# Kernel tuning notes

Measured on AMD Instinct MI355X. Metric: run time of the kernel, lower is better.

The kernel has to match this reference:

```python
import jax, jax.numpy as jnp
import numpy as np

B, H, W = 32, 128, 128
NA = 9            # number of anchors
STRIDE = 16.0
CLS_THRESH = 0.95
MAX_IOU = 0.1
NUM_PROP = 10
NEG = -1e9        # sentinel for suppressed / below-threshold scores


def setup_inputs() -> dict:
    key = jax.random.key(0)
    inputs = jax.random.normal(key, (B, H, W, NA * 4 + NA + 1), dtype=jnp.float32)
    anchors = jnp.array([[0.5, 32.0], [1.0, 32.0], [2.0, 32.0],
                         [0.5, 64.0], [1.0, 64.0], [2.0, 64.0],
                         [0.5, 128.0], [1.0, 128.0], [2.0, 128.0]], dtype=jnp.float32)
    return {"inputs": inputs, "anchors": anchors}


def _decode(inputs, anchors):
    b, h, w, c = inputs.shape
    cls = inputs[..., -1]
    # zero out 1-pixel border (the tf.pad'ed cancel matrix)
    border = jnp.zeros((h, w), inputs.dtype).at[1:-1, 1:-1].set(1.0)
    cls = cls * border
    a_reg = inputs[..., -10:-1]           # [B,H,W,9]
    bbox_reg = inputs[..., :-10]          # [B,H,W,36]
    a_idx = jnp.argmax(a_reg, axis=-1)    # [B,H,W] best anchor per position
    # gather the 4 deltas of the chosen anchor: channels a_idx*4 .. a_idx*4+3
    gidx = a_idx[..., None] * 4 + jnp.arange(4)
    deltas = jnp.take_along_axis(bbox_reg, gidx, axis=-1)          # [B,H,W,4]
    anc = anchors[a_idx].astype(jnp.float32)                       # [B,H,W,2]
    # anchor box: center x from column, center y from row, height=anc[:,1], width=anc[:,1]/anc[:,0]
    ax = (jnp.arange(w, dtype=jnp.float32)[None, :] + 0.5) * STRIDE  # [1,W]
    ay = (jnp.arange(h, dtype=jnp.float32)[:, None] + 0.5) * STRIDE  # [H,1]
    a0 = jnp.broadcast_to(ax, (h, w))[None]                          # [1,H,W]
    a1 = jnp.broadcast_to(ay, (h, w))[None]
    a2 = anc[..., 1]
    a3 = anc[..., 1] / anc[..., 0]
    b0 = deltas[..., 0] * a2 + a0
    b1 = deltas[..., 1] * a3 + a1
    b2 = jnp.exp(deltas[..., 2]) * a2
    b3 = jnp.exp(deltas[..., 3]) * a3
    bboxes = jnp.stack([b0, b1, b2, b3], axis=-1)                    # [B,H,W,4]
    coords = jnp.stack([b1 - b3 / 2, b0 - b2 / 2,
                        b1 + b3 / 2, b0 + b2 / 2], axis=-1)          # [y1,x1,y2,x2]
    scores = jnp.where(cls > CLS_THRESH, cls, NEG)                   # mask below-threshold
    n = h * w
    return (bboxes.reshape(b, n, 4), coords.reshape(b, n, 4), scores.reshape(b, n))


def _nms_one(boxes, coords, scores):
    # greedy NMS, equivalent to tf.image.non_max_suppression over the valid candidates
    n = scores.shape[0]
    area = jnp.maximum(coords[:, 2] - coords[:, 0], 0.0) * jnp.maximum(coords[:, 3] - coords[:, 1], 0.0)
    idx_range = jnp.arange(n)

    def body(i, state):
        sc, out = state
        j = jnp.argmax(sc)
        ok = sc[j] > NEG / 2
        sel = coords[j]
        iy1 = jnp.maximum(coords[:, 0], sel[0])
        ix1 = jnp.maximum(coords[:, 1], sel[1])
        iy2 = jnp.minimum(coords[:, 2], sel[2])
        ix2 = jnp.minimum(coords[:, 3], sel[3])
        inter = jnp.maximum(iy2 - iy1, 0.0) * jnp.maximum(ix2 - ix1, 0.0)
        area_s = jnp.maximum(sel[2] - sel[0], 0.0) * jnp.maximum(sel[3] - sel[1], 0.0)
        iou = inter / (area + area_s - inter + 1e-10)
        suppress = (iou > MAX_IOU) | (idx_range == j)
        sc = jnp.where(ok & suppress, NEG, sc)
        out = out.at[i].set(jnp.where(ok, boxes[j], jnp.zeros(4, boxes.dtype)))
        return sc, out

    out0 = jnp.zeros((NUM_PROP, 4), boxes.dtype)
    _, out = jax.lax.fori_loop(0, NUM_PROP, body, (scores, out0))
    return out


def _forward(inputs, anchors):
    bboxes, coords, scores = _decode(inputs, anchors)
    return jax.vmap(_nms_one)(bboxes, coords, scores)   # [B, NUM_PROP, 4]


def reference(inputs, anchors):
    return _forward(inputs, anchors)
```

## Files before the change

kernel.cpp:

```cpp
#include <hip/hip_runtime.h>
#include <math.h>

#define BB 32
#define HH 128
#define WW 128
#define NA 9
#define CCH 46
#define NPIX (HH*WW)
#define STRIDE_F 16.0f
#define CLS_T 0.95f
#define MAX_IOU_F 0.1f
#define NUM_PROP 10
#define NEGV -1000000000.0f

#define TILE_PIX 256
#define TILE_FLOATS (TILE_PIX * CCH)
#define TILE_VEC (TILE_FLOATS / 4)

#define NSHARD 8
#define NREG (BB * NSHARD)
#define MAXPER 20
#define MMAX (MAXPER * 256)

#define GLL16(gp, lp)                                                          \
  __builtin_amdgcn_global_load_lds(                                            \
      (__attribute__((address_space(1))) void*)(gp),                           \
      (__attribute__((address_space(3))) void*)(lp), 16, 0, 0)

__global__ __launch_bounds__(256, 3) void decode_kernel(
    const float* __restrict__ in, const float* __restrict__ anchors,
    char* __restrict__ counters, float* __restrict__ sc_comp,
    float4* __restrict__ co_comp, int capS)
{
  __shared__ float s_in[TILE_FLOATS];

  int tid = threadIdx.x;
  int tile = blockIdx.x;
  int g0 = tile * TILE_PIX;

  const float4* srcv = (const float4*)(in + (size_t)g0 * CCH);
  float4* dstv = (float4*)s_in;
#pragma unroll
  for (int i = 0; i < 12; ++i) {
    int k = tid + i * 256;
    if (k < TILE_VEC)
      GLL16(srcv + k, dstv + k);
  }
  __syncthreads();

  int b = tile >> 6;
  int shard = tile & (NSHARD - 1);
  int region = b * NSHARD + shard;

  int g = g0 + tid;
  int p = g & (NPIX - 1);
  int h = p >> 7;
  int w = p & (WW - 1);
  const float* px = s_in + tid * CCH;

  float cls = px[45];
  bool interior = (h >= 1) && (h <= HH - 2) && (w >= 1) && (w <= WW - 2);
  bool cand = interior && (cls > CLS_T);

  unsigned long long mask = __ballot(cand);
  if (!cand) return;

  int ai = 0; float av = px[36];
#pragma unroll
  for (int c = 1; c < NA; ++c) { float v = px[36 + c]; if (v > av) { av = v; ai = c; } }

  float d0 = px[ai * 4 + 0], d1 = px[ai * 4 + 1];
  float d2 = px[ai * 4 + 2], d3 = px[ai * 4 + 3];
  float ratio = anchors[ai * 2 + 0], sz = anchors[ai * 2 + 1];
  float a2 = sz, a3 = sz / ratio;
  float ax = ((float)w + 0.5f) * STRIDE_F;
  float ay = ((float)h + 0.5f) * STRIDE_F;
  float b0 = d0 * a2 + ax;
  float b1 = d1 * a3 + ay;
  float b2 = expf(d2) * a2;
  float b3 = expf(d3) * a3;
  float4 co = make_float4(b1 - 0.5f * b3, b0 - 0.5f * b2,
                          b1 + 0.5f * b3, b0 + 0.5f * b2);

  int lane = tid & 63;
  int prefix = __popcll(mask & ((1ull << lane) - 1ull));
  int leader = __ffsll((unsigned long long)mask) - 1;
  int total = __popcll(mask);
  int base = 0;
  int* cnt = (int*)(counters + (size_t)region * 128);
  if (lane == leader) base = atomicAdd(cnt, total);
  base = __shfl(base, leader);
  int slot = base + prefix;
  if (slot < capS) {
    size_t gi = (size_t)region * capS + slot;
    sc_comp[gi] = cls;
    co_comp[gi] = co;
  }
}

__global__ __launch_bounds__(256, 1) void nms_kernel(
    const char* __restrict__ counters, const float* __restrict__ sc_comp,
    const float4* __restrict__ co_comp, float* __restrict__ out, int capS)
{
  __shared__ int   s_off[NSHARD + 1];
  __shared__ float s_rv[4];
  __shared__ int   s_rk[4];
  __shared__ float s_rc[4][4];
  __shared__ float s_ra[4];
  __shared__ float s_jv;
  __shared__ int   s_jk;
  __shared__ float s_selc[4];
  __shared__ float s_area;

  int b = blockIdx.x, tid = threadIdx.x;

  if (tid == 0) {
    int acc = 0;
    s_off[0] = 0;
#pragma unroll
    for (int s = 0; s < NSHARD; ++s) {
      int c = *(const int*)(counters + (size_t)(b * NSHARD + s) * 128);
      if (c > capS) c = capS;
      acc += c;
      s_off[s + 1] = acc;
    }
  }
  __syncthreads();
  int M = s_off[NSHARD];
  if (M > MMAX) M = MMAX;

  float  sc[MAXPER];
  float4 co[MAXPER];
  float  ar[MAXPER];
#pragma unroll
  for (int r = 0; r < MAXPER; ++r) {
    int k = r * 256 + tid;
    if (k < M) {
      int s = 0;
#pragma unroll
      for (int t = 1; t < NSHARD; ++t) if (k >= s_off[t]) s = t;
      int gi = (b * NSHARD + s) * capS + (k - s_off[s]);
      sc[r] = sc_comp[gi];
      co[r] = co_comp[gi];
      ar[r] = fmaxf(co[r].z - co[r].x, 0.f) * fmaxf(co[r].w - co[r].y, 0.f);
    } else {
      sc[r] = NEGV; co[r] = make_float4(0.f, 0.f, 0.f, 0.f); ar[r] = 0.f;
    }
  }

  for (int it = 0; it < NUM_PROP; ++it) {
    float bv = -INFINITY; int bk = 0x7fffffff;
    float4 bc = make_float4(0.f, 0.f, 0.f, 0.f); float ba = 0.f;
#pragma unroll
    for (int r = 0; r < MAXPER; ++r) {
      if (sc[r] > bv) { bv = sc[r]; bk = r * 256 + tid; bc = co[r]; ba = ar[r]; }
    }
    for (int off = 32; off > 0; off >>= 1) {
      float ov = __shfl_down(bv, off);
      int   ok_ = __shfl_down(bk, off);
      float ocx = __shfl_down(bc.x, off), ocy = __shfl_down(bc.y, off);
      float ocz = __shfl_down(bc.z, off), ocw = __shfl_down(bc.w, off);
      float oa = __shfl_down(ba, off);
      if (ov > bv || (ov == bv && ok_ < bk)) {
        bv = ov; bk = ok_; ba = oa;
        bc.x = ocx; bc.y = ocy; bc.z = ocz; bc.w = ocw;
      }
    }
    int wv = tid >> 6;
    if ((tid & 63) == 0) {
      s_rv[wv] = bv; s_rk[wv] = bk;
      s_rc[wv][0] = bc.x; s_rc[wv][1] = bc.y; s_rc[wv][2] = bc.z; s_rc[wv][3] = bc.w;
      s_ra[wv] = ba;
    }
    __syncthreads();
    if (tid == 0) {
      float fv = s_rv[0]; int fk = s_rk[0]; int fw = 0;
#pragma unroll
      for (int q = 1; q < 4; ++q) {
        if (s_rv[q] > fv || (s_rv[q] == fv && s_rk[q] < fk)) { fv = s_rv[q]; fk = s_rk[q]; fw = q; }
      }
      s_jv = fv; s_jk = fk;
      s_selc[0] = s_rc[fw][0]; s_selc[1] = s_rc[fw][1];
      s_selc[2] = s_rc[fw][2]; s_selc[3] = s_rc[fw][3];
      s_area = s_ra[fw];
    }
    __syncthreads();
    float jv = s_jv;
    bool okq = jv > (NEGV * 0.5f);

    if (okq) {
      int jk = s_jk;
      float sy1 = s_selc[0], sx1 = s_selc[1], sy2 = s_selc[2], sx2 = s_selc[3];
      float sarea = s_area;
#pragma unroll
      for (int r = 0; r < MAXPER; ++r) {
        float4 c = co[r];
        float iy1 = fmaxf(c.x, sy1);
        float ix1 = fmaxf(c.y, sx1);
        float iy2 = fminf(c.z, sy2);
        float ix2 = fminf(c.w, sx2);
        float inter = fmaxf(iy2 - iy1, 0.f) * fmaxf(ix2 - ix1, 0.f);
        float iou = inter / (ar[r] + sarea - inter + 1e-10f);
        if (iou > MAX_IOU_F || (r * 256 + tid) == jk) sc[r] = NEGV;
      }
      if (tid == 0) {
        float* o = out + (size_t)(b * NUM_PROP + it) * 4;
        o[0] = 0.5f * (sx1 + sx2);
        o[1] = 0.5f * (sy1 + sy2);
        o[2] = sx2 - sx1;
        o[3] = sy2 - sy1;
      }
    } else if (tid == 0) {
      float* o = out + (size_t)(b * NUM_PROP + it) * 4;
      o[0] = 0.f; o[1] = 0.f; o[2] = 0.f; o[3] = 0.f;
    }
    __syncthreads();
  }
}

extern "C" void kernel_launch(void* const* d_in, const int* in_sizes, int n_in,
                              void* d_out, int out_size, void* d_ws, size_t ws_size,
                              hipStream_t stream) {
  const float* in      = (const float*)d_in[0];
  const float* anchors = (const float*)d_in[1];
  float* out = (float*)d_out;

  char* ws = (char*)d_ws;
  size_t cnt_bytes = (size_t)NREG * 128;
  size_t avail = (ws_size > cnt_bytes) ? (ws_size - cnt_bytes) : 0;
  long long capS_ll = (long long)(avail / ((size_t)NREG * 20));
  int capS = (int)((capS_ll > 1024) ? 1024 : capS_ll);
  if (capS < 1) capS = 1;

  float4* co_comp = (float4*)(ws + cnt_bytes);
  size_t co_bytes = (size_t)NREG * capS * 16;
  float*  sc_comp = (float*)(ws + cnt_bytes + co_bytes);

  hipMemsetAsync(ws, 0, cnt_bytes, stream);

  decode_kernel<<<(BB * NPIX) / TILE_PIX, 256, 0, stream>>>(
      in, anchors, ws, sc_comp, co_comp, capS);
  nms_kernel<<<BB, 256, 0, stream>>>(
      ws, sc_comp, co_comp, out, capS);
}
```

Baseline: 177.8 us.

## Replace atomic sharded compaction with per-wave fixed slots and in-NMS prefix scan

The decode kernel now writes each wave's candidates into a fixed 64-entry slot per wave and records a per-wave count, which removes the global atomics and the memset launch. The NMS kernel, now 512 threads, runs a shared-memory prefix scan over the 256 wave counts of its batch, compacts candidates into LDS, and fetches the selected box from LDS instead of shuffling coordinates through the reduction. This trades atomic contention and an extra launch for a serial per-thread copy loop, a larger fixed-size workspace, and a 5120-candidate cap.

New measurement: 171.5 us. 1.04x faster.

```diff
diff --git a/kernel.cpp b/kernel.cpp
--- a/kernel.cpp
+++ b/kernel.cpp
@@ -17,10 +17,13 @@
 #define TILE_FLOATS (TILE_PIX * CCH)
 #define TILE_VEC (TILE_FLOATS / 4)
 
-#define NSHARD 8
-#define NREG (BB * NSHARD)
-#define MAXPER 20
-#define MMAX (MAXPER * 256)
+#define NTILE (BB * NPIX / TILE_PIX)
+#define NWAVES (NTILE * 4)
+#define WSLOT 64
+
+#define NMS_T 512
+#define MAXPER 10
+#define MMAX (MAXPER * NMS_T)
 
 #define GLL16(gp, lp)                                                          \
   __builtin_amdgcn_global_load_lds(                                            \
@@ -29,8 +32,8 @@
 
 __global__ __launch_bounds__(256, 3) void decode_kernel(
     const float* __restrict__ in, const float* __restrict__ anchors,
-    char* __restrict__ counters, float* __restrict__ sc_comp,
-    float4* __restrict__ co_comp, int capS)
+    int* __restrict__ wcnt, float* __restrict__ sc_comp,
+    float4* __restrict__ co_comp)
 {
   __shared__ float s_in[TILE_FLOATS];
 
@@ -47,10 +50,6 @@
       GLL16(srcv + k, dstv + k);
   }
   __syncthreads();
-
-  int b = tile >> 6;
-  int shard = tile & (NSHARD - 1);
-  int region = b * NSHARD + shard;
 
   int g = g0 + tid;
   int p = g & (NPIX - 1);
@@ -63,6 +62,11 @@
   bool cand = interior && (cls > CLS_T);
 
   unsigned long long mask = __ballot(cand);
+  int lane = tid & 63;
+  int waveid = tile * 4 + (tid >> 6);
+  int total = __popcll(mask);
+  if (lane == 0) wcnt[waveid] = total;
+
   if (!cand) return;
 
   int ai = 0; float av = px[36];
@@ -82,66 +86,57 @@
   float4 co = make_float4(b1 - 0.5f * b3, b0 - 0.5f * b2,
                           b1 + 0.5f * b3, b0 + 0.5f * b2);
 
-  int lane = tid & 63;
   int prefix = __popcll(mask & ((1ull << lane) - 1ull));
-  int leader = __ffsll((unsigned long long)mask) - 1;
-  int total = __popcll(mask);
-  int base = 0;
-  int* cnt = (int*)(counters + (size_t)region * 128);
-  if (lane == leader) base = atomicAdd(cnt, total);
-  base = __shfl(base, leader);
-  int slot = base + prefix;
-  if (slot < capS) {
-    size_t gi = (size_t)region * capS + slot;
-    sc_comp[gi] = cls;
-    co_comp[gi] = co;
-  }
+  int slot = waveid * WSLOT + prefix;
+  sc_comp[slot] = cls;
+  co_comp[slot] = co;
 }
 
-__global__ __launch_bounds__(256, 1) void nms_kernel(
-    const char* __restrict__ counters, const float* __restrict__ sc_comp,
-    const float4* __restrict__ co_comp, float* __restrict__ out, int capS)
+__global__ __launch_bounds__(NMS_T, 1) void nms_kernel(
+    const int* __restrict__ wcnt, const float* __restrict__ sc_comp,
+    const float4* __restrict__ co_comp, float* __restrict__ out)
 {
-  __shared__ int   s_off[NSHARD + 1];
-  __shared__ float s_rv[4];
-  __shared__ int   s_rk[4];
-  __shared__ float s_rc[4][4];
-  __shared__ float s_ra[4];
-  __shared__ float s_jv;
-  __shared__ int   s_jk;
-  __shared__ float s_selc[4];
-  __shared__ float s_area;
+  __shared__ float  s_sc[MMAX];
+  __shared__ float4 s_co[MMAX];
+  __shared__ int    s_tmp[256];
+  __shared__ float  s_rv[8];
+  __shared__ int    s_rk[8];
+  __shared__ float  s_jv;
+  __shared__ int    s_jk;
 
   int b = blockIdx.x, tid = threadIdx.x;
 
-  if (tid == 0) {
-    int acc = 0;
-    s_off[0] = 0;
-#pragma unroll
-    for (int s = 0; s < NSHARD; ++s) {
-      int c = *(const int*)(counters + (size_t)(b * NSHARD + s) * 128);
-      if (c > capS) c = capS;
-      acc += c;
-      s_off[s + 1] = acc;
-    }
-  }
+  int c = 0;
+  if (tid < 256) { c = wcnt[b * 256 + tid]; s_tmp[tid] = c; }
   __syncthreads();
-  int M = s_off[NSHARD];
-  if (M > MMAX) M = MMAX;
+  for (int d = 1; d < 256; d <<= 1) {
+    int v = 0;
+    if (tid < 256) { v = s_tmp[tid]; if (tid >= d) v += s_tmp[tid - d]; }
+    __syncthreads();
+    if (tid < 256) s_tmp[tid] = v;
+    __syncthreads();
+  }
+  if (tid < 256) {
+    int excl = s_tmp[tid] - c;
+    const float*  sp = sc_comp + (size_t)(b * 256 + tid) * WSLOT;
+    const float4* cp = co_comp + (size_t)(b * 256 + tid) * WSLOT;
+    for (int i = 0; i < c; ++i) {
+      int d = excl + i;
+      if (d < MMAX) { s_sc[d] = sp[i]; s_co[d] = cp[i]; }
+    }
+  }
+  __syncthreads();
+  int M = s_tmp[255]; if (M > MMAX) M = MMAX;
 
   float  sc[MAXPER];
   float4 co[MAXPER];
   float  ar[MAXPER];
 #pragma unroll
   for (int r = 0; r < MAXPER; ++r) {
-    int k = r * 256 + tid;
+    int k = r * NMS_T + tid;
     if (k < M) {
-      int s = 0;
-#pragma unroll
-      for (int t = 1; t < NSHARD; ++t) if (k >= s_off[t]) s = t;
-      int gi = (b * NSHARD + s) * capS + (k - s_off[s]);
-      sc[r] = sc_comp[gi];
-      co[r] = co_comp[gi];
+      sc[r] = s_sc[k];
+      co[r] = s_co[k];
       ar[r] = fmaxf(co[r].z - co[r].x, 0.f) * fmaxf(co[r].w - co[r].y, 0.f);
     } else {
       sc[r] = NEGV; co[r] = make_float4(0.f, 0.f, 0.f, 0.f); ar[r] = 0.f;
@@ -150,39 +145,25 @@
 
   for (int it = 0; it < NUM_PROP; ++it) {
     float bv = -INFINITY; int bk = 0x7fffffff;
-    float4 bc = make_float4(0.f, 0.f, 0.f, 0.f); float ba = 0.f;
 #pragma unroll
     for (int r = 0; r < MAXPER; ++r) {
-      if (sc[r] > bv) { bv = sc[r]; bk = r * 256 + tid; bc = co[r]; ba = ar[r]; }
+      if (sc[r] > bv) { bv = sc[r]; bk = r * NMS_T + tid; }
     }
     for (int off = 32; off > 0; off >>= 1) {
       float ov = __shfl_down(bv, off);
       int   ok_ = __shfl_down(bk, off);
-      float ocx = __shfl_down(bc.x, off), ocy = __shfl_down(bc.y, off);
-      float ocz = __shfl_down(bc.z, off), ocw = __shfl_down(bc.w, off);
-      float oa = __shfl_down(ba, off);
-      if (ov > bv || (ov == bv && ok_ < bk)) {
-        bv = ov; bk = ok_; ba = oa;
-        bc.x = ocx; bc.y = ocy; bc.z = ocz; bc.w = ocw;
-      }
+      if (ov > bv || (ov == bv && ok_ < bk)) { bv = ov; bk = ok_; }
     }
     int wv = tid >> 6;
-    if ((tid & 63) == 0) {
-      s_rv[wv] = bv; s_rk[wv] = bk;
-      s_rc[wv][0] = bc.x; s_rc[wv][1] = bc.y; s_rc[wv][2] = bc.z; s_rc[wv][3] = bc.w;
-      s_ra[wv] = ba;
-    }
+    if ((tid & 63) == 0) { s_rv[wv] = bv; s_rk[wv] = bk; }
     __syncthreads();
     if (tid == 0) {
-      float fv = s_rv[0]; int fk = s_rk[0]; int fw = 0;
-#pragma unroll
-      for (int q = 1; q < 4; ++q) {
-        if (s_rv[q] > fv || (s_rv[q] == fv && s_rk[q] < fk)) { fv = s_rv[q]; fk = s_rk[q]; fw = q; }
+      float fv = s_rv[0]; int fk = s_rk[0];
+#pragma unroll
+      for (int q = 1; q < 8; ++q) {
+        if (s_rv[q] > fv || (s_rv[q] == fv && s_rk[q] < fk)) { fv = s_rv[q]; fk = s_rk[q]; }
       }
       s_jv = fv; s_jk = fk;
-      s_selc[0] = s_rc[fw][0]; s_selc[1] = s_rc[fw][1];
-      s_selc[2] = s_rc[fw][2]; s_selc[3] = s_rc[fw][3];
-      s_area = s_ra[fw];
     }
     __syncthreads();
     float jv = s_jv;
@@ -190,18 +171,19 @@
 
     if (okq) {
       int jk = s_jk;
-      float sy1 = s_selc[0], sx1 = s_selc[1], sy2 = s_selc[2], sx2 = s_selc[3];
-      float sarea = s_area;
+      float4 selc = s_co[jk];
+      float sy1 = selc.x, sx1 = selc.y, sy2 = selc.z, sx2 = selc.w;
+      float sarea = fmaxf(sy2 - sy1, 0.f) * fmaxf(sx2 - sx1, 0.f);
 #pragma unroll
       for (int r = 0; r < MAXPER; ++r) {
-        float4 c = co[r];
-        float iy1 = fmaxf(c.x, sy1);
-        float ix1 = fmaxf(c.y, sx1);
-        float iy2 = fminf(c.z, sy2);
-        float ix2 = fminf(c.w, sx2);
+        float4 cc = co[r];
+        float iy1 = fmaxf(cc.x, sy1);
+        float ix1 = fmaxf(cc.y, sx1);
+        float iy2 = fminf(cc.z, sy2);
+        float ix2 = fminf(cc.w, sx2);
         float inter = fmaxf(iy2 - iy1, 0.f) * fmaxf(ix2 - ix1, 0.f);
         float iou = inter / (ar[r] + sarea - inter + 1e-10f);
-        if (iou > MAX_IOU_F || (r * 256 + tid) == jk) sc[r] = NEGV;
+        if (iou > MAX_IOU_F || (r * NMS_T + tid) == jk) sc[r] = NEGV;
       }
       if (tid == 0) {
         float* o = out + (size_t)(b * NUM_PROP + it) * 4;
@@ -226,20 +208,10 @@
   float* out = (float*)d_out;
 
   char* ws = (char*)d_ws;
-  size_t cnt_bytes = (size_t)NREG * 128;
-  size_t avail = (ws_size > cnt_bytes) ? (ws_size - cnt_bytes) : 0;
-  long long capS_ll = (long long)(avail / ((size_t)NREG * 20));
-  int capS = (int)((capS_ll > 1024) ? 1024 : capS_ll);
-  if (capS < 1) capS = 1;
-
-  float4* co_comp = (float4*)(ws + cnt_bytes);
-  size_t co_bytes = (size_t)NREG * capS * 16;
-  float*  sc_comp = (float*)(ws + cnt_bytes + co_bytes);
-
-  hipMemsetAsync(ws, 0, cnt_bytes, stream);
-
-  decode_kernel<<<(BB * NPIX) / TILE_PIX, 256, 0, stream>>>(
-      in, anchors, ws, sc_comp, co_comp, capS);
-  nms_kernel<<<BB, 256, 0, stream>>>(
-      ws, sc_comp, co_comp, out, capS);
+  int*    wcnt    = (int*)ws;
+  float4* co_comp = (float4*)(ws + (size_t)NWAVES * 4);
+  float*  sc_comp = (float*)(ws + (size_t)NWAVES * 4 + (size_t)NWAVES * WSLOT * 16);
+
+  decode_kernel<<<NTILE, 256, 0, stream>>>(in, anchors, wcnt, sc_comp, co_comp);
+  nms_kernel<<<BB, NMS_T, 0, stream>>>(wcnt, sc_comp, co_comp, out);
 }
```
